# Kernel optimization log

Hardware: AMD Instinct MI355X
Metric: run time of the kernel (lower is better)

## Reference

```python
import jax, jax.numpy as jnp
from jax import lax
import numpy as np

NEG = jnp.float32(-1e9)


def monotonic_alignment_search(logp, text_lengths, mel_lengths):
    """Glow-TTS style MAS. logp: [B, Tt, Tm] (log_softmax over text axis).
    Returns integer durations [B, Tt] summing to mel_lengths per batch."""
    B, Tt, Tm = logp.shape
    i_range = jnp.arange(Tt)
    text_mask = i_range[None, :] < text_lengths[:, None]            # [B, Tt]
    logp = jnp.where(text_mask[:, :, None], logp, NEG)

    # ---- forward DP over mel frames: Q[i,j] = logp[i,j] + max(Q[i,j-1], Q[i-1,j-1])
    q0 = jnp.where(i_range[None, :] == 0, logp[:, :, 0], NEG)        # [B, Tt]

    def fwd(q, lp_j):
        q_shift = jnp.concatenate([jnp.full((B, 1), NEG), q[:, :-1]], axis=1)
        take_diag = q_shift > q                                      # came from i-1
        q_new = lp_j + jnp.maximum(q, q_shift)
        return q_new, take_diag

    _, choices = lax.scan(fwd, q0, jnp.moveaxis(logp[:, :, 1:], 2, 0))  # [Tm-1, B, Tt]
    choices = jnp.concatenate([jnp.zeros((1, B, Tt), bool), choices], axis=0)  # align j

    # ---- backtrack from (text_len-1, mel_len-1) down to j=0
    b_idx = jnp.arange(B)

    def bwd(i, j):
        active = j < mel_lengths                                     # [B]
        dur_inc = (active[:, None] & (i_range[None, :] == i[:, None]))
        ch = choices[j, b_idx, i]                                    # [B] bool
        i_new = jnp.where(active & (j > 0), i - ch.astype(i.dtype), i)
        return i_new, dur_inc

    i0 = text_lengths - 1
    _, durs = lax.scan(bwd, i0, jnp.arange(Tm - 1, -1, -1))
    return durs.sum(0).astype(jnp.int32)                             # [B, Tt]


def length_regulate(h_text, durations, mel_lengths, Tm):
    """Expand h_text [B,Tt,D] by durations [B,Tt] to [B,Tm,D]."""
    B, Tt, D = h_text.shape
    cum = jnp.cumsum(durations, axis=1)                              # [B, Tt]
    j = jnp.arange(Tm)
    idx = (cum[:, None, :] <= j[None, :, None]).sum(-1)              # [B, Tm]
    idx = jnp.clip(idx, 0, Tt - 1)
    h_exp = jnp.take_along_axis(h_text, idx[:, :, None], axis=1)     # [B, Tm, D]
    mel_mask = j[None, :] < mel_lengths[:, None]
    return h_exp * mel_mask[:, :, None].astype(h_exp.dtype)


def setup_inputs() -> dict:
    B, Tt, Tm, D, M = 32, 512, 2048, 512, 80
    k = jax.random.split(jax.random.key(0), 6)
    return {
        "h_text": jax.random.normal(k[0], (B, Tt, D), jnp.float32),
        "mel": jax.random.normal(k[1], (B, M, Tm), jnp.float32),
        "text_lengths": jax.random.randint(k[2], (B,), 256, Tt + 1, jnp.int32),
        "mel_lengths": jax.random.randint(k[3], (B,), 1024, Tm + 1, jnp.int32),
        "w_proj": jax.random.normal(k[4], (D, M), jnp.float32) * 0.02,
        "b_proj": jnp.zeros((D,), jnp.float32),
        "log_dur_pred": jax.random.normal(k[5], (B, Tt), jnp.float32) * 0.5,
    }


def reference(h_text, mel, text_lengths, mel_lengths, w_proj, b_proj, log_dur_pred):
    B, Tt, D = h_text.shape
    Tm = mel.shape[2]

    # mel_proj = Linear(n_mels -> d_model) on mel.transpose(1,2)
    mel_proj = jnp.einsum('bmt,dm->btd', mel, w_proj) + b_proj       # [B, Tm, D]

    # alignment scores + masked log_softmax over text axis
    attn = jnp.einsum('btd,bsd->bts', h_text, mel_proj)              # [B, Tt, Tm]
    text_mask = jnp.arange(Tt)[None, :] >= text_lengths[:, None]
    mel_mask = jnp.arange(Tm)[None, :] >= mel_lengths[:, None]
    attn = jnp.where(text_mask[:, :, None], NEG, attn)
    attn = jnp.where(mel_mask[:, None, :], NEG, attn)
    logp = jax.nn.log_softmax(attn, axis=1)

    durations = monotonic_alignment_search(logp, text_lengths, mel_lengths)

    # duration loss (masked sum-MSE in log domain)
    dur_mask = (jnp.arange(Tt)[None, :] < text_lengths[:, None]).astype(jnp.float32)
    log_dur_gt = jnp.log(jnp.clip(durations.astype(jnp.float32), 1.0, None))
    diff = log_dur_pred * dur_mask - log_dur_gt * dur_mask
    dur_loss = jnp.sum(diff * diff) / jnp.sum(dur_mask)

    h_expanded = length_regulate(h_text, durations, mel_lengths, Tm)  # [B, Tm, D]
    return (h_expanded, dur_loss, durations)
```

## Files before the change

kernel.cpp:

```cpp
#include <hip/hip_runtime.h>
#include <math.h>

#define Bn 32
#define TT 512
#define TM 2048
#define DD 512
#define MMp 80
#define NEGF (-1.0e9f)

constexpr size_t LOSS_OFF = (size_t)Bn * TM * DD;
constexpr size_t DUR_OFF  = LOSS_OFF + 1;

__global__ __launch_bounds__(256) void k0_wtx(const float* __restrict__ w,
                                              const float* __restrict__ bias,
                                              float* __restrict__ wTx) {
    int m = blockIdx.x;
    for (int d = threadIdx.x; d < DD; d += 256) {
        float v = 0.f;
        if (m < 80) v = w[d * 80 + m];
        else if (m == 80) v = bias[d];
        wTx[m * DD + d] = v;
    }
}

__global__ __launch_bounds__(256) void k1_hw(const float* __restrict__ h_text,
                                             const float* __restrict__ wTx,
                                             float* __restrict__ hwX) {
    int bid = blockIdx.x;
    int b = bid >> 3;
    int i0 = (bid & 7) * 64;
    int t = threadIdx.x;
    int tr = t & 15, tc = t >> 4;
    __shared__ __align__(16) float Asub[64 * 68];
    __shared__ __align__(16) float Bsub[96 * 68];
    float acc[4][6];
#pragma unroll
    for (int a = 0; a < 4; ++a)
#pragma unroll
        for (int c = 0; c < 6; ++c) acc[a][c] = 0.f;

    for (int d0 = 0; d0 < DD; d0 += 64) {
        __syncthreads();
#pragma unroll
        for (int p = 0; p < 4; ++p) {
            int lin = p * 256 + t;
            int r = lin >> 4, dq = lin & 15;
            *(float4*)&Asub[r * 68 + dq * 4] =
                *(const float4*)&h_text[((size_t)(b * TT + i0 + r)) * DD + d0 + dq * 4];
        }
#pragma unroll
        for (int p = 0; p < 6; ++p) {
            int lin = p * 256 + t;
            int cc = lin >> 4, dq = lin & 15;
            *(float4*)&Bsub[cc * 68 + dq * 4] =
                *(const float4*)&wTx[(size_t)cc * DD + d0 + dq * 4];
        }
        __syncthreads();
#pragma unroll
        for (int dd = 0; dd < 16; ++dd) {
            float4 a[4], bb[6];
#pragma unroll
            for (int ri = 0; ri < 4; ++ri)
                a[ri] = *(const float4*)&Asub[(tr * 4 + ri) * 68 + dd * 4];
#pragma unroll
            for (int ci = 0; ci < 6; ++ci)
                bb[ci] = *(const float4*)&Bsub[(tc * 6 + ci) * 68 + dd * 4];
#pragma unroll
            for (int ri = 0; ri < 4; ++ri)
#pragma unroll
                for (int ci = 0; ci < 6; ++ci) {
                    acc[ri][ci] += a[ri].x * bb[ci].x;
                    acc[ri][ci] += a[ri].y * bb[ci].y;
                    acc[ri][ci] += a[ri].z * bb[ci].z;
                    acc[ri][ci] += a[ri].w * bb[ci].w;
                }
        }
    }
#pragma unroll
    for (int ri = 0; ri < 4; ++ri)
#pragma unroll
        for (int ci = 0; ci < 6; ++ci)
            hwX[((size_t)b * 96 + tc * 6 + ci) * DD + i0 + tr * 4 + ri] = acc[ri][ci];
}

__global__ __launch_bounds__(256) void k2_attn(const float* __restrict__ hwX,
                                               const float* __restrict__ mel,
                                               const int* __restrict__ tlen,
                                               const int* __restrict__ mlen,
                                               float* __restrict__ logpT) {
    const int b = blockIdx.y;
    const int ml = mlen[b];
    const int j0 = blockIdx.x * 32;
    if (j0 >= ml) return;
    const int tl = tlen[b];
    const int tid = threadIdx.x;
    const int ig = tid >> 2;
    const int jg = tid & 3;

    __shared__ __align__(16) float hwS[16 * 512];
    __shared__ __align__(16) float melS[16 * 32];
    __shared__ float red[32 * 64];
    __shared__ float colmax[32];
    __shared__ float lsum[32];

    float acc[8][8];
#pragma unroll
    for (int a = 0; a < 8; ++a)
#pragma unroll
        for (int c = 0; c < 8; ++c) acc[a][c] = 0.f;

    for (int mc = 0; mc < 80; mc += 16) {
        __syncthreads();
#pragma unroll
        for (int p = 0; p < 8; ++p) {
            int lin = p * 256 + tid;
            int mm = lin >> 7, iq = lin & 127;
            *(float4*)&hwS[mm * 512 + iq * 4] =
                *(const float4*)&hwX[((size_t)b * 96 + mc + mm) * DD + iq * 4];
        }
#pragma unroll
        for (int p = 0; p < 2; ++p) {
            int lin = p * 256 + tid;
            int mm = lin >> 5, jj = lin & 31;
            melS[lin] = mel[((size_t)b * 80 + mc + mm) * TM + j0 + jj];
        }
        __syncthreads();
#pragma unroll
        for (int mm = 0; mm < 16; ++mm) {
            float4 a0 = *(const float4*)&hwS[mm * 512 + ig * 8];
            float4 a1 = *(const float4*)&hwS[mm * 512 + ig * 8 + 4];
            float4 b0 = *(const float4*)&melS[mm * 32 + jg * 8];
            float4 b1 = *(const float4*)&melS[mm * 32 + jg * 8 + 4];
            float av[8] = {a0.x, a0.y, a0.z, a0.w, a1.x, a1.y, a1.z, a1.w};
            float bv[8] = {b0.x, b0.y, b0.z, b0.w, b1.x, b1.y, b1.z, b1.w};
#pragma unroll
            for (int ii = 0; ii < 8; ++ii)
#pragma unroll
                for (int jj = 0; jj < 8; ++jj) acc[ii][jj] += av[ii] * bv[jj];
        }
    }
    float4 h0 = *(const float4*)&hwX[((size_t)b * 96 + 80) * DD + ig * 8];
    float4 h1 = *(const float4*)&hwX[((size_t)b * 96 + 80) * DD + ig * 8 + 4];
    float hb[8] = {h0.x, h0.y, h0.z, h0.w, h1.x, h1.y, h1.z, h1.w};
#pragma unroll
    for (int ii = 0; ii < 8; ++ii) {
        bool valid = (ig * 8 + ii) < tl;
#pragma unroll
        for (int jj = 0; jj < 8; ++jj)
            acc[ii][jj] = valid ? (acc[ii][jj] + hb[ii]) : NEGF;
    }
    __syncthreads();
#pragma unroll
    for (int jj = 0; jj < 8; ++jj) {
        float m = acc[0][jj];
#pragma unroll
        for (int ii = 1; ii < 8; ++ii) m = fmaxf(m, acc[ii][jj]);
        red[(jg * 8 + jj) * 64 + ig] = m;
    }
    __syncthreads();
    if (tid < 32) {
        float m = red[tid * 64];
        for (int g = 1; g < 64; ++g) m = fmaxf(m, red[tid * 64 + g]);
        colmax[tid] = m;
    }
    __syncthreads();
#pragma unroll
    for (int jj = 0; jj < 8; ++jj) {
        float cm = colmax[jg * 8 + jj];
        float s = 0.f;
#pragma unroll
        for (int ii = 0; ii < 8; ++ii) s += expf(acc[ii][jj] - cm);
        red[(jg * 8 + jj) * 64 + ig] = s;
    }
    __syncthreads();
    if (tid < 32) {
        float s = 0.f;
        for (int g = 0; g < 64; ++g) s += red[tid * 64 + g];
        lsum[tid] = logf(s);
    }
    __syncthreads();
#pragma unroll
    for (int jj = 0; jj < 8; ++jj) {
        int j = j0 + jg * 8 + jj;
        if (j < ml) {
            float cm = colmax[jg * 8 + jj], ls = lsum[jg * 8 + jj];
            float o[8];
#pragma unroll
            for (int ii = 0; ii < 8; ++ii) {
                int i = ig * 8 + ii;
                o[ii] = (i < tl) ? ((acc[ii][jj] - cm) - ls) : NEGF;
            }
            float* dst = &logpT[((size_t)b * TM + j) * TT + ig * 8];
            *(float4*)dst = make_float4(o[0], o[1], o[2], o[3]);
            *(float4*)(dst + 4) = make_float4(o[4], o[5], o[6], o[7]);
        }
    }
}

#define BCOLS 8
#define NBATCH 256

typedef float vf4 __attribute__((ext_vector_type(4)));

#define SB0() __builtin_amdgcn_sched_barrier(0)

__device__ __forceinline__ float dpp_shr1(float old, float src) {
    return __int_as_float(__builtin_amdgcn_update_dpp(
        __float_as_int(old), __float_as_int(src), 0x138, 0xF, 0xF, false));
}

__global__ __launch_bounds__(64, 1) void k3_dp(const float* __restrict__ logpT,
                                               const int* __restrict__ tlen,
                                               const int* __restrict__ mlen,
                                               unsigned* __restrict__ gwords,
                                               int* __restrict__ idxmap,
                                               float* __restrict__ dOut) {
    const int b = blockIdx.x;
    const int lane = threadIdx.x;
    const int tl = tlen[b];
    const int ml = mlen[b];
    __shared__ int durs[TT];
#pragma unroll
    for (int k = 0; k < 8; ++k) durs[lane * 8 + k] = 0;

    const float* colbase = logpT + (size_t)b * TM * TT;
    unsigned* gwb = gwords + (size_t)b * TT * 64;

    float q[8];
    unsigned accb[8];
#pragma unroll
    for (int k = 0; k < 8; ++k) { q[k] = NEGF; accb[k] = 0u; }
    if (lane == 0) q[0] = colbase[0];

    unsigned* gp = gwb + lane * 8 * 64;
    int jj = 1;
    const float* lanebase = colbase + lane * 8;

    vf4 ra0[BCOLS], rb0[BCOLS], ra1[BCOLS], rb1[BCOLS];

#define ISSUE(nb_, ra_, rb_) do {                                              \
        const float* g_ = lanebase + ((size_t)(1 + (nb_) * 8)) * 512;          \
        _Pragma("unroll")                                                      \
        for (int p_ = 0; p_ < BCOLS; ++p_) {                                   \
            ra_[p_] = *(const vf4*)(g_ + (size_t)p_ * 512);                    \
            rb_[p_] = *(const vf4*)(g_ + (size_t)p_ * 512 + 4);                \
        }                                                                      \
    } while (0)

#define STEPS(ra_, rb_) do {                                                   \
        _Pragma("unroll")                                                      \
        for (int p_ = 0; p_ < BCOLS; ++p_) {                                   \
            float lp_[8] = {ra_[p_][0], ra_[p_][1], ra_[p_][2], ra_[p_][3],    \
                            rb_[p_][0], rb_[p_][1], rb_[p_][2], rb_[p_][3]};   \
            float nb_[8];                                                      \
            nb_[0] = dpp_shr1(NEGF, q[7]);                                     \
            _Pragma("unroll")                                                  \
            for (int k_ = 1; k_ < 8; ++k_) nb_[k_] = q[k_ - 1];                \
            const unsigned m32_ = 1u << (jj & 31);                             \
            _Pragma("unroll")                                                  \
            for (int k_ = 0; k_ < 8; ++k_) {                                   \
                if (nb_[k_] > q[k_]) accb[k_] |= m32_;                         \
                q[k_] = lp_[k_] + fmaxf(q[k_], nb_[k_]);                       \
            }                                                                  \
            if ((jj & 31) == 31) {                \
                _Pragma("unroll")                                              \
                for (int k_ = 0; k_ < 8; ++k_) {                               \
                    gp[k_ * 64] = accb[k_]; accb[k_] = 0u;                     \
                }                                                              \
                gp += 1;                                                       \
            }                                                                  \
            ++jj;                                                              \
        }                                                                      \
    } while (0)

    ISSUE(0, ra0, rb0);
    ISSUE(1, ra1, rb1);
    for (int n = 0; n < NBATCH; n += 2) {
        SB0();
        STEPS(ra0, rb0);
        SB0();
        ISSUE(n + 2, ra0, rb0);
        SB0();
        STEPS(ra1, rb1);
        SB0();
        ISSUE(n + 3, ra1, rb1);
    }
    SB0();
#undef ISSUE
#undef STEPS

    __threadfence();
    __syncthreads();

    {
        int i = tl - 1;
        int j = ml - 1;
        unsigned r0, r1, r2, r3, r4, r5, r6, r7;
        {
            int a0 = tl - 1, a1 = tl - 2, a2 = tl - 3, a3 = tl - 4;
            int a4 = tl - 5, a5 = tl - 6, a6 = tl - 7, a7 = tl - 8;
            a1 = a1 < 0 ? 0 : a1; a2 = a2 < 0 ? 0 : a2; a3 = a3 < 0 ? 0 : a3;
            a4 = a4 < 0 ? 0 : a4; a5 = a5 < 0 ? 0 : a5; a6 = a6 < 0 ? 0 : a6;
            a7 = a7 < 0 ? 0 : a7;
            r0 = gwb[a0 * 64 + lane]; r1 = gwb[a1 * 64 + lane];
            r2 = gwb[a2 * 64 + lane]; r3 = gwb[a3 * 64 + lane];
            r4 = gwb[a4 * 64 + lane]; r5 = gwb[a5 * 64 + lane];
            r6 = gwb[a6 * 64 + lane]; r7 = gwb[a7 * 64 + lane];
        }
        int nf = tl - 9;
        int guard = TT + 2;
        while (guard-- > 0) {
            unsigned w = r0;
            r0 = r1; r1 = r2; r2 = r3; r3 = r4; r4 = r5; r5 = r6; r6 = r7;
            {
                int rf = (nf < 0) ? 0 : nf;
                r7 = gwb[rf * 64 + lane];
                --nf;
            }
            int jw = j >> 5, rr = j & 31;
            unsigned topmask = (rr == 31) ? 0xFFFFFFFFu : ((1u << (rr + 1)) - 1u);
            unsigned wm = (lane < jw) ? w : ((lane == jw) ? (w & topmask) : 0u);
            unsigned long long bal = __ballot(wm != 0u);
            if (bal == 0ull) {
                if (lane == 0) durs[i] = j + 1;
                break;
            }
            int hl = 63 - __clzll(bal);
            unsigned whl = (unsigned)__builtin_amdgcn_readlane((int)wm, hl);
            int jp = (hl << 5) + (31 - __clz(whl));
            if (lane == 0) durs[i] = j - jp + 1;
            j = jp - 1;
            if (--i < 0) break;
        }
    }
    __syncthreads();

    int d[8], pre[8];
    int run = 0;
#pragma unroll
    for (int k = 0; k < 8; ++k) { d[k] = durs[lane * 8 + k]; pre[k] = run; run += d[k]; }
    int v = run;
#pragma unroll
    for (int off = 1; off < 64; off <<= 1) {
        int n = __shfl_up(v, off);
        if (lane >= off) v += n;
    }
    int base = v - run;
#pragma unroll
    for (int k = 0; k < 8; ++k) {
        int i = lane * 8 + k;
        dOut[DUR_OFF + (size_t)b * TT + i] = (float)d[k];
        int st = base + pre[k];
        int en = st + d[k];
        if (en > TM) en = TM;
        if (st < 0) st = 0;
        for (int t2 = st; t2 < en; ++t2) idxmap[b * TM + t2] = i;
    }
}

__global__ __launch_bounds__(128) void k4_expand(const float* __restrict__ h_text,
                                                 const int* __restrict__ idxmap,
                                                 const int* __restrict__ mlen,
                                                 float* __restrict__ dOut) {
    int bid = blockIdx.x;
    int b = bid >> 11;
    int j = bid & (TM - 1);
    int t = threadIdx.x;
    float4* orow = (float4*)dOut + (size_t)bid * 128;
    if (j < mlen[b]) {
        int i = idxmap[bid] & (TT - 1);
        const float4* hrow = (const float4*)h_text + ((size_t)(b * TT + i)) * 128;
        orow[t] = hrow[t];
    } else {
        orow[t] = make_float4(0.f, 0.f, 0.f, 0.f);
    }
}

__global__ __launch_bounds__(256) void k5_loss(const float* __restrict__ pred,
                                               const int* __restrict__ tlen,
                                               float* __restrict__ dOut) {
    __shared__ float rs[256];
    __shared__ int rc[256];
    int t = threadIdx.x;
    float s = 0.f;
    int c = 0;
    for (int idx = t; idx < Bn * TT; idx += 256) {
        int b = idx >> 9, i = idx & 511;
        if (i < tlen[b]) {
            float dv = dOut[DUR_OFF + idx];
            float lg = logf(fmaxf(dv, 1.0f));
            float df = pred[idx] - lg;
            s += df * df;
            c += 1;
        }
    }
    rs[t] = s; rc[t] = c;
    __syncthreads();
    for (int off = 128; off > 0; off >>= 1) {
        if (t < off) { rs[t] += rs[t + off]; rc[t] += rc[t + off]; }
        __syncthreads();
    }
    if (t == 0) dOut[LOSS_OFF] = rs[0] / (float)rc[0];
}

extern "C" void kernel_launch(void* const* d_in, const int* in_sizes, int n_in,
                              void* d_out, int out_size, void* d_ws, size_t ws_size,
                              hipStream_t stream) {
    const float* h_text = (const float*)d_in[0];
    const float* mel    = (const float*)d_in[1];
    const int*   tlen   = (const int*)d_in[2];
    const int*   mlen   = (const int*)d_in[3];
    const float* w      = (const float*)d_in[4];
    const float* bias   = (const float*)d_in[5];
    const float* pred   = (const float*)d_in[6];
    float* out = (float*)d_out;

    float*    logpT  = (float*)d_ws;
    float*    hwX    = logpT + (size_t)Bn * TM * TT;
    float*    wTx    = hwX + (size_t)Bn * 96 * DD;
    unsigned* gwords = (unsigned*)(wTx + 96 * DD);
    int*      idxmap = (int*)(gwords + (size_t)Bn * TT * 64);

    k0_wtx<<<dim3(96), dim3(256), 0, stream>>>(w, bias, wTx);
    k1_hw<<<dim3(256), dim3(256), 0, stream>>>(h_text, wTx, hwX);
    k2_attn<<<dim3(64, 32), dim3(256), 0, stream>>>(hwX, mel, tlen, mlen, logpT);
    k3_dp<<<dim3(32), dim3(64), 0, stream>>>(logpT, tlen, mlen, gwords, idxmap, out);
    k4_expand<<<dim3(Bn * TM), dim3(128), 0, stream>>>(h_text, idxmap, mlen, out);
    k5_loss<<<dim3(1), dim3(256), 0, stream>>>(pred, tlen, out);
}
```

Before: 727.6 us.

## Stage DP log-prob columns through LDS ring via direct global-to-LDS DMA

The serial MAS forward DP kernel now streams log-prob columns into a double-buffered LDS ring with global_load_lds instead of holding them in large register batches. Each lane now owns two interleaved 4-row strips (rows 4*lane and 256+4*lane) rather than one 8-row strip, and a DPP rotate carries the boundary value between the halves. The goal is to cut register pressure and hide global load latency behind the sequential recurrence. In exchange it adds LDS reads and hand-written waitcnt synchronisation, and the fixed vmcnt(32) value has to match the number of DMAs issued per batch.

```diff
diff --git a/kernel.cpp b/kernel.cpp
--- a/kernel.cpp
+++ b/kernel.cpp
@@ -197,16 +197,26 @@
     }
 }
 
-#define BCOLS 8
-#define NBATCH 256
+#define KVB 16
+#define NKB 128
 
 typedef float vf4 __attribute__((ext_vector_type(4)));
+
+__device__ __forceinline__ void lds_dma16(const float* g, float* l) {
+    __builtin_amdgcn_global_load_lds((const __attribute__((address_space(1))) void*)g,
+                                     (__attribute__((address_space(3))) void*)l,
+                                     16, 0, 0);
+}
 
 #define SB0() __builtin_amdgcn_sched_barrier(0)
 
 __device__ __forceinline__ float dpp_shr1(float old, float src) {
     return __int_as_float(__builtin_amdgcn_update_dpp(
         __float_as_int(old), __float_as_int(src), 0x138, 0xF, 0xF, false));
+}
+__device__ __forceinline__ float dpp_ror1(float src) {
+    return __int_as_float(__builtin_amdgcn_update_dpp(
+        __float_as_int(src), __float_as_int(src), 0x13C, 0xF, 0xF, false));
 }
 
 __global__ __launch_bounds__(64, 1) void k3_dp(const float* __restrict__ logpT,
@@ -219,75 +229,105 @@
     const int lane = threadIdx.x;
     const int tl = tlen[b];
     const int ml = mlen[b];
+
+    __shared__ __align__(16) float ring[2][KVB][512];
     __shared__ int durs[TT];
-#pragma unroll
-    for (int k = 0; k < 8; ++k) durs[lane * 8 + k] = 0;
+    for (int idx = lane; idx < TT; idx += 64) durs[idx] = 0;
 
     const float* colbase = logpT + (size_t)b * TM * TT;
     unsigned* gwb = gwords + (size_t)b * TT * 64;
 
-    float q[8];
-    unsigned accb[8];
-#pragma unroll
-    for (int k = 0; k < 8; ++k) { q[k] = NEGF; accb[k] = 0u; }
-    if (lane == 0) q[0] = colbase[0];
-
-    unsigned* gp = gwb + lane * 8 * 64;
+    float qa[4], qb[4];
+    unsigned accA[4], accB[4];
+#pragma unroll
+    for (int k = 0; k < 4; ++k) { qa[k] = NEGF; qb[k] = NEGF; accA[k] = 0u; accB[k] = 0u; }
+    float q00 = colbase[0];
+    asm volatile("" :: "v"(q00));
+    if (lane == 0) qa[0] = q00;
+
+    unsigned* gpA = gwb + (size_t)(4 * lane) * 64;
+    unsigned* gpB = gwb + (size_t)(256 + 4 * lane) * 64;
+    int woff = 0;
     int jj = 1;
-    const float* lanebase = colbase + lane * 8;
-
-    vf4 ra0[BCOLS], rb0[BCOLS], ra1[BCOLS], rb1[BCOLS];
-
-#define ISSUE(nb_, ra_, rb_) do {                                              \
-        const float* g_ = lanebase + ((size_t)(1 + (nb_) * 8)) * 512;          \
+    const int lane4 = lane * 4;
+
+#define DMA_BATCH(nb_, slot_) do {                                             \
+        const float* src_ = colbase + (size_t)(1 + (nb_) * KVB) * 512 + lane4; \
+        float* dst_ = &ring[slot_][0][0];                                      \
         _Pragma("unroll")                                                      \
-        for (int p_ = 0; p_ < BCOLS; ++p_) {                                   \
-            ra_[p_] = *(const vf4*)(g_ + (size_t)p_ * 512);                    \
-            rb_[p_] = *(const vf4*)(g_ + (size_t)p_ * 512 + 4);                \
+        for (int c_ = 0; c_ < KVB; ++c_) {                                     \
+            lds_dma16(src_ + c_ * 512,       dst_ + c_ * 512);                 \
+            lds_dma16(src_ + c_ * 512 + 256, dst_ + c_ * 512 + 256);           \
         }                                                                      \
     } while (0)
 
-#define STEPS(ra_, rb_) do {                                                   \
+#define COL1(la_, lb_) do {                                                    \
+        float wrap_ = dpp_ror1(qa[3]);                   \
+        float nA0_ = dpp_shr1(NEGF, qa[3]);         \
+        float nB0_ = dpp_shr1(wrap_, qb[3]);           \
+        float nA_[4], nB_[4];                                                  \
+        nA_[0] = nA0_; nB_[0] = nB0_;                                          \
         _Pragma("unroll")                                                      \
-        for (int p_ = 0; p_ < BCOLS; ++p_) {                                   \
-            float lp_[8] = {ra_[p_][0], ra_[p_][1], ra_[p_][2], ra_[p_][3],    \
-                            rb_[p_][0], rb_[p_][1], rb_[p_][2], rb_[p_][3]};   \
-            float nb_[8];                                                      \
-            nb_[0] = dpp_shr1(NEGF, q[7]);                                     \
+        for (int k_ = 1; k_ < 4; ++k_) { nA_[k_] = qa[k_ - 1]; nB_[k_] = qb[k_ - 1]; } \
+        const unsigned m32_ = 1u << (jj & 31);                                 \
+        _Pragma("unroll")                                                      \
+        for (int k_ = 0; k_ < 4; ++k_) {                                       \
+            if (nA_[k_] > qa[k_]) accA[k_] |= m32_;                            \
+            qa[k_] = la_[k_] + fmaxf(qa[k_], nA_[k_]);                         \
+            if (nB_[k_] > qb[k_]) accB[k_] |= m32_;                            \
+            qb[k_] = lb_[k_] + fmaxf(qb[k_], nB_[k_]);                         \
+        }                                                                      \
+        if ((jj & 31) == 31) {                              \
             _Pragma("unroll")                                                  \
-            for (int k_ = 1; k_ < 8; ++k_) nb_[k_] = q[k_ - 1];                \
-            const unsigned m32_ = 1u << (jj & 31);                             \
-            _Pragma("unroll")                                                  \
-            for (int k_ = 0; k_ < 8; ++k_) {                                   \
-                if (nb_[k_] > q[k_]) accb[k_] |= m32_;                         \
-                q[k_] = lp_[k_] + fmaxf(q[k_], nb_[k_]);                       \
+            for (int k_ = 0; k_ < 4; ++k_) {                                   \
+                gpA[k_ * 64 + woff] = accA[k_]; accA[k_] = 0u;                 \
+                gpB[k_ * 64 + woff] = accB[k_]; accB[k_] = 0u;                 \
             }                                                                  \
-            if ((jj & 31) == 31) {                \
-                _Pragma("unroll")                                              \
-                for (int k_ = 0; k_ < 8; ++k_) {                               \
-                    gp[k_ * 64] = accb[k_]; accb[k_] = 0u;                     \
-                }                                                              \
-                gp += 1;                                                       \
-            }                                                                  \
-            ++jj;                                                              \
+            ++woff;                                                            \
+        }                                                                      \
+        ++jj;                                                                  \
+    } while (0)
+
+#define READG(slab_, c0_, ga_, gb_) do {                                       \
+        _Pragma("unroll")                                                      \
+        for (int p_ = 0; p_ < 4; ++p_) {                                       \
+            ga_[p_] = *(const vf4*)&slab_[(c0_ + p_) * 512 + lane4];           \
+            gb_[p_] = *(const vf4*)&slab_[(c0_ + p_) * 512 + 256 + lane4];     \
         }                                                                      \
     } while (0)
 
-    ISSUE(0, ra0, rb0);
-    ISSUE(1, ra1, rb1);
-    for (int n = 0; n < NBATCH; n += 2) {
+#define COMPG(ga_, gb_) do {                                                   \
+        _Pragma("unroll")                                                      \
+        for (int p_ = 0; p_ < 4; ++p_) COL1(ga_[p_], gb_[p_]);                 \
+    } while (0)
+
+    DMA_BATCH(0, 0);
+    DMA_BATCH(1, 1);
+
+    for (int n = 0; n < NKB; ++n) {
+        asm volatile("s_waitcnt vmcnt(32)" ::: "memory");
         SB0();
-        STEPS(ra0, rb0);
+        const float* slab = &ring[n & 1][0][0];
+        vf4 xA[4], xB[4], yA[4], yB[4];
+        READG(slab, 0, xA, xB);
+        READG(slab, 4, yA, yB);
+        COMPG(xA, xB);
+        READG(slab, 8, xA, xB);
+        COMPG(yA, yB);
+        READG(slab, 12, yA, yB);
+        COMPG(xA, xB);
+        COMPG(yA, yB);
         SB0();
-        ISSUE(n + 2, ra0, rb0);
+        asm volatile("s_waitcnt lgkmcnt(0)" ::: "memory");
         SB0();
-        STEPS(ra1, rb1);
+        if (n + 2 < NKB) DMA_BATCH(n + 2, n & 1);
         SB0();
-        ISSUE(n + 3, ra1, rb1);
-    }
-    SB0();
-#undef ISSUE
-#undef STEPS
+    }
+    asm volatile("s_waitcnt vmcnt(0) lgkmcnt(0)" ::: "memory");
+#undef DMA_BATCH
+#undef COL1
+#undef READG
+#undef COMPG
 
     __threadfence();
     __syncthreads();
```

Result: slower. 829.4 us (+14.0%).

## Add a helper prefetch wave to warm cache ahead of the DP wave

Applied to the files above, without the earlier changes.

Launches the DP kernel with two waves per block. The second wave touches logp columns a few batches ahead of the DP wave so that they are already in cache, and both waves sync with a barrier each iteration. A dummy reduction is written to scratch so the prefetch loads are not removed. The aim is to hide global memory latency on the serial DP scan, at the cost of a per-iteration block barrier that could stall the critical wave.

```diff
diff --git a/kernel.cpp b/kernel.cpp
--- a/kernel.cpp
+++ b/kernel.cpp
@@ -199,6 +199,7 @@
 
 #define BCOLS 8
 #define NBATCH 256
+#define NITER (NBATCH / 2)
 
 typedef float vf4 __attribute__((ext_vector_type(4)));
 
@@ -209,19 +210,21 @@
         __float_as_int(old), __float_as_int(src), 0x138, 0xF, 0xF, false));
 }
 
-__global__ __launch_bounds__(64, 1) void k3_dp(const float* __restrict__ logpT,
-                                               const int* __restrict__ tlen,
-                                               const int* __restrict__ mlen,
-                                               unsigned* __restrict__ gwords,
-                                               int* __restrict__ idxmap,
-                                               float* __restrict__ dOut) {
+__global__ __launch_bounds__(128, 1) void k3_dp(const float* __restrict__ logpT,
+                                                const int* __restrict__ tlen,
+                                                const int* __restrict__ mlen,
+                                                unsigned* __restrict__ gwords,
+                                                int* __restrict__ idxmap,
+                                                float* __restrict__ scratch,
+                                                float* __restrict__ dOut) {
     const int b = blockIdx.x;
-    const int lane = threadIdx.x;
+    const int tid = threadIdx.x;
+    const int wid = tid >> 6;
+    const int lane = tid & 63;
     const int tl = tlen[b];
     const int ml = mlen[b];
     __shared__ int durs[TT];
-#pragma unroll
-    for (int k = 0; k < 8; ++k) durs[lane * 8 + k] = 0;
+    for (int idx = tid; idx < TT; idx += 128) durs[idx] = 0;
 
     const float* colbase = logpT + (size_t)b * TM * TT;
     unsigned* gwb = gwords + (size_t)b * TT * 64;
@@ -230,13 +233,15 @@
     unsigned accb[8];
 #pragma unroll
     for (int k = 0; k < 8; ++k) { q[k] = NEGF; accb[k] = 0u; }
-    if (lane == 0) q[0] = colbase[0];
+    if (wid == 0 && lane == 0) q[0] = colbase[0];
 
     unsigned* gp = gwb + lane * 8 * 64;
     int jj = 1;
     const float* lanebase = colbase + lane * 8;
 
     vf4 ra0[BCOLS], rb0[BCOLS], ra1[BCOLS], rb1[BCOLS];
+    float tA[4] = {0, 0, 0, 0}, tB[4] = {0, 0, 0, 0}, tC[4] = {0, 0, 0, 0};
+    float fold = 0.f;
 
 #define ISSUE(nb_, ra_, rb_) do {                                              \
         const float* g_ = lanebase + ((size_t)(1 + (nb_) * 8)) * 512;          \
@@ -273,88 +278,110 @@
         }                                                                      \
     } while (0)
 
-    ISSUE(0, ra0, rb0);
-    ISSUE(1, ra1, rb1);
-    for (int n = 0; n < NBATCH; n += 2) {
-        SB0();
-        STEPS(ra0, rb0);
-        SB0();
-        ISSUE(n + 2, ra0, rb0);
-        SB0();
-        STEPS(ra1, rb1);
-        SB0();
-        ISSUE(n + 3, ra1, rb1);
-    }
-    SB0();
+#define TOUCH(nb_, ts_) do {                                                   \
+        fold += ts_[0] + ts_[1] + ts_[2] + ts_[3];                             \
+        const float* g_ = colbase + (size_t)(1 + (nb_) * 8) * 512 + lane * 32; \
+        ts_[0] = g_[0];                                                        \
+        ts_[1] = g_[2048];                                                     \
+        ts_[2] = g_[4096];                                                     \
+        ts_[3] = g_[6144];                                                     \
+    } while (0)
+
+    if (wid == 0) {
+        ISSUE(0, ra0, rb0);
+        ISSUE(1, ra1, rb1);
+    }
+    for (int it = 0; it < NITER; ++it) {
+        if (wid == 0) {
+            SB0();
+            STEPS(ra0, rb0);
+            SB0();
+            ISSUE(2 * it + 2, ra0, rb0);
+            SB0();
+            STEPS(ra1, rb1);
+            SB0();
+            ISSUE(2 * it + 3, ra1, rb1);
+            SB0();
+        } else {
+            int s = it % 3;
+            if (s == 0)      TOUCH(2 * it + 6, tA);
+            else if (s == 1) TOUCH(2 * it + 6, tB);
+            else             TOUCH(2 * it + 6, tC);
+        }
+        __builtin_amdgcn_s_barrier();
+    }
 #undef ISSUE
 #undef STEPS
+#undef TOUCH
+    if (wid == 1 && lane == 0) scratch[b] = fold;
 
     __threadfence();
     __syncthreads();
 
-    {
-        int i = tl - 1;
-        int j = ml - 1;
-        unsigned r0, r1, r2, r3, r4, r5, r6, r7;
+    if (wid == 0) {
         {
-            int a0 = tl - 1, a1 = tl - 2, a2 = tl - 3, a3 = tl - 4;
-            int a4 = tl - 5, a5 = tl - 6, a6 = tl - 7, a7 = tl - 8;
-            a1 = a1 < 0 ? 0 : a1; a2 = a2 < 0 ? 0 : a2; a3 = a3 < 0 ? 0 : a3;
-            a4 = a4 < 0 ? 0 : a4; a5 = a5 < 0 ? 0 : a5; a6 = a6 < 0 ? 0 : a6;
-            a7 = a7 < 0 ? 0 : a7;
-            r0 = gwb[a0 * 64 + lane]; r1 = gwb[a1 * 64 + lane];
-            r2 = gwb[a2 * 64 + lane]; r3 = gwb[a3 * 64 + lane];
-            r4 = gwb[a4 * 64 + lane]; r5 = gwb[a5 * 64 + lane];
-            r6 = gwb[a6 * 64 + lane]; r7 = gwb[a7 * 64 + lane];
-        }
-        int nf = tl - 9;
-        int guard = TT + 2;
-        while (guard-- > 0) {
-            unsigned w = r0;
-            r0 = r1; r1 = r2; r2 = r3; r3 = r4; r4 = r5; r5 = r6; r6 = r7;
+            int i = tl - 1;
+            int j = ml - 1;
+            unsigned r0, r1, r2, r3, r4, r5, r6, r7;
             {
-                int rf = (nf < 0) ? 0 : nf;
-                r7 = gwb[rf * 64 + lane];
-                --nf;
+                int a0 = tl - 1, a1 = tl - 2, a2 = tl - 3, a3 = tl - 4;
+                int a4 = tl - 5, a5 = tl - 6, a6 = tl - 7, a7 = tl - 8;
+                a1 = a1 < 0 ? 0 : a1; a2 = a2 < 0 ? 0 : a2; a3 = a3 < 0 ? 0 : a3;
+                a4 = a4 < 0 ? 0 : a4; a5 = a5 < 0 ? 0 : a5; a6 = a6 < 0 ? 0 : a6;
+                a7 = a7 < 0 ? 0 : a7;
+                r0 = gwb[a0 * 64 + lane]; r1 = gwb[a1 * 64 + lane];
+                r2 = gwb[a2 * 64 + lane]; r3 = gwb[a3 * 64 + lane];
+                r4 = gwb[a4 * 64 + lane]; r5 = gwb[a5 * 64 + lane];
+                r6 = gwb[a6 * 64 + lane]; r7 = gwb[a7 * 64 + lane];
             }
-            int jw = j >> 5, rr = j & 31;
-            unsigned topmask = (rr == 31) ? 0xFFFFFFFFu : ((1u << (rr + 1)) - 1u);
-            unsigned wm = (lane < jw) ? w : ((lane == jw) ? (w & topmask) : 0u);
-            unsigned long long bal = __ballot(wm != 0u);
-            if (bal == 0ull) {
-                if (lane == 0) durs[i] = j + 1;
-                break;
+            int nf = tl - 9;
+            int guard = TT + 2;
+            while (guard-- > 0) {
+                unsigned w = r0;
+                r0 = r1; r1 = r2; r2 = r3; r3 = r4; r4 = r5; r5 = r6; r6 = r7;
+                {
+                    int rf = (nf < 0) ? 0 : nf;
+                    r7 = gwb[rf * 64 + lane];
+                    --nf;
+                }
+                int jw = j >> 5, rr = j & 31;
+                unsigned topmask = (rr == 31) ? 0xFFFFFFFFu : ((1u << (rr + 1)) - 1u);
+                unsigned wm = (lane < jw) ? w : ((lane == jw) ? (w & topmask) : 0u);
+                unsigned long long bal = __ballot(wm != 0u);
+                if (bal == 0ull) {
+                    if (lane == 0) durs[i] = j + 1;
+                    break;
+                }
+                int hl = 63 - __clzll(bal);
+                unsigned whl = (unsigned)__builtin_amdgcn_readlane((int)wm, hl);
+                int jp = (hl << 5) + (31 - __clz(whl));
+                if (lane == 0) durs[i] = j - jp + 1;
+                j = jp - 1;
+                if (--i < 0) break;
             }
-            int hl = 63 - __clzll(bal);
-            unsigned whl = (unsigned)__builtin_amdgcn_readlane((int)wm, hl);
-            int jp = (hl << 5) + (31 - __clz(whl));
-            if (lane == 0) durs[i] = j - jp + 1;
-            j = jp - 1;
-            if (--i < 0) break;
-        }
-    }
-    __syncthreads();
-
-    int d[8], pre[8];
-    int run = 0;
-#pragma unroll
-    for (int k = 0; k < 8; ++k) { d[k] = durs[lane * 8 + k]; pre[k] = run; run += d[k]; }
-    int v = run;
-#pragma unroll
-    for (int off = 1; off < 64; off <<= 1) {
-        int n = __shfl_up(v, off);
-        if (lane >= off) v += n;
-    }
-    int base = v - run;
-#pragma unroll
-    for (int k = 0; k < 8; ++k) {
-        int i = lane * 8 + k;
-        dOut[DUR_OFF + (size_t)b * TT + i] = (float)d[k];
-        int st = base + pre[k];
-        int en = st + d[k];
-        if (en > TM) en = TM;
-        if (st < 0) st = 0;
-        for (int t2 = st; t2 < en; ++t2) idxmap[b * TM + t2] = i;
+        }
+
+        int d[8], pre[8];
+        int run = 0;
+#pragma unroll
+        for (int k = 0; k < 8; ++k) { d[k] = durs[lane * 8 + k]; pre[k] = run; run += d[k]; }
+        int v = run;
+#pragma unroll
+        for (int off = 1; off < 64; off <<= 1) {
+            int n = __shfl_up(v, off);
+            if (lane >= off) v += n;
+        }
+        int base = v - run;
+#pragma unroll
+        for (int k = 0; k < 8; ++k) {
+            int i = lane * 8 + k;
+            dOut[DUR_OFF + (size_t)b * TT + i] = (float)d[k];
+            int st = base + pre[k];
+            int en = st + d[k];
+            if (en > TM) en = TM;
+            if (st < 0) st = 0;
+            for (int t2 = st; t2 < en; ++t2) idxmap[b * TM + t2] = i;
+        }
     }
 }
 
@@ -424,7 +451,7 @@
     k0_wtx<<<dim3(96), dim3(256), 0, stream>>>(w, bias, wTx);
     k1_hw<<<dim3(256), dim3(256), 0, stream>>>(h_text, wTx, hwX);
     k2_attn<<<dim3(64, 32), dim3(256), 0, stream>>>(hwX, mel, tlen, mlen, logpT);
-    k3_dp<<<dim3(32), dim3(64), 0, stream>>>(logpT, tlen, mlen, gwords, idxmap, out);
+    k3_dp<<<dim3(32), dim3(128), 0, stream>>>(logpT, tlen, mlen, gwords, idxmap, hwX, out);
     k4_expand<<<dim3(Bn * TM), dim3(128), 0, stream>>>(h_text, idxmap, mlen, out);
     k5_loss<<<dim3(1), dim3(256), 0, stream>>>(pred, tlen, out);
 }
```

Measured after the change: 824.2 us. +13.3%, slower.
